# Kernel tuning notes

Hardware: AMD Instinct MI355X
Metric: run time of the kernel (lower is better)

## Reference

```python
import jax, jax.numpy as jnp
import numpy as np

N_ITER = 3  # routing iterations (init kwarg n_iter)


def _squash_elemwise(s):
    # Original squash sums squares over dim=-1, but s_j has a trailing
    # singleton dim there, so it degenerates to an elementwise map:
    # s^2/(1+s^2) * s/|s| == s*|s|/(1+s^2).
    return s * jnp.abs(s) / (1.0 + s * s)


def setup_inputs() -> dict:
    key = jax.random.key(0)
    k1, k2 = jax.random.split(key)
    B, R, C, O, I = 256, 1152, 10, 16, 8
    x = jax.random.normal(k1, (B, R, I), dtype=jnp.float32)
    W = jax.random.normal(k2, (R, C, O, I), dtype=jnp.float32)  # nn.Parameter (leading 1 dropped)
    return {"x": x, "W": W}


def reference(x, W):
    # u_hat[b,r,c,o] = sum_i W[r,c,o,i] * x[b,r,i]
    u_hat = jnp.einsum('rcoi,bri->brco', W, x)  # [B,R,C,O]
    R, C = u_hat.shape[1], u_hat.shape[2]
    b = jnp.zeros((R, C), dtype=u_hat.dtype)  # routing logits, shared across batch
    v = None
    for it in range(N_ITER):
        c = jax.nn.softmax(b, axis=0)                     # softmax over routes (dim=1 orig)
        s = jnp.einsum('rc,brco->bco', c, u_hat)          # weighted sum over routes
        v = _squash_elemwise(s)                           # [B,C,O]
        if it < N_ITER - 1:
            # agreement, mean over batch (b_ij is [1,R,C,1] in original)
            b = b + jnp.einsum('brco,bco->brc', u_hat, v).mean(axis=0)
    return v[..., None]  # matches v_j.squeeze(1): [B, n_capsules, out_ch, 1]
```

## Files before the change

kernel.cpp:

```cpp
#include <hip/hip_runtime.h>
#include <math.h>

namespace {
constexpr int NB = 256;
constexpr int NR = 1152;
constexpr int NC = 10;
constexpr int NO = 16;
constexpr int NI = 8;
constexpr int K1 = NR * NI;
constexpr int NN = NC * NO;
constexpr int KS = 8;
constexpr int KC = K1 / KS;
constexpr int RPB = NR / KS;
}

using s16x8 = __attribute__((ext_vector_type(8))) short;
using f32x4 = __attribute__((ext_vector_type(4))) float;

__device__ __forceinline__ ushort f2bf(float f) {
    uint u = __float_as_uint(f);
    uint r = (u + 0x7FFFu + ((u >> 16) & 1u)) >> 16;
    return (ushort)r;
}

__device__ __forceinline__ s16x8 pack8(float4 a0, float4 a1) {
    s16x8 r;
    r[0] = (short)f2bf(a0.x); r[1] = (short)f2bf(a0.y);
    r[2] = (short)f2bf(a0.z); r[3] = (short)f2bf(a0.w);
    r[4] = (short)f2bf(a1.x); r[5] = (short)f2bf(a1.y);
    r[6] = (short)f2bf(a1.z); r[7] = (short)f2bf(a1.w);
    return r;
}

__device__ __forceinline__ s16x8 pack8s(float4 a0, float4 a1, float cr) {
    s16x8 r;
    r[0] = (short)f2bf(a0.x * cr); r[1] = (short)f2bf(a0.y * cr);
    r[2] = (short)f2bf(a0.z * cr); r[3] = (short)f2bf(a0.w * cr);
    r[4] = (short)f2bf(a1.x * cr); r[5] = (short)f2bf(a1.y * cr);
    r[6] = (short)f2bf(a1.z * cr); r[7] = (short)f2bf(a1.w * cr);
    return r;
}

template <bool FIRST>
__global__ __launch_bounds__(256) void k_a(const float* __restrict__ x,
                                           const float* __restrict__ W,
                                           ushort* __restrict__ Wb,
                                           const float* __restrict__ bbuf,
                                           float* __restrict__ spart,
                                           ushort* __restrict__ xTbf) {
    const int m0 = blockIdx.x * 16;
    const int c  = blockIdx.y;
    const int ks = blockIdx.z;
    const int tid = threadIdx.x;
    const int w = tid >> 6, l = tid & 63;

    __shared__ float red[4][16][16];
    __shared__ float crs[RPB];
    __shared__ float sred[4], sred2[4];

    if constexpr (FIRST) {
        __shared__ __align__(16) ushort T[32][264];
        const int bid = blockIdx.x + 16 * blockIdx.y + 160 * blockIdx.z;
        if (bid < K1 / 32) {
            const int k0 = bid * 32;
            #pragma unroll
            for (int j = 0; j < 8; ++j) {
                int f  = j * 256 + tid;
                int b  = f >> 3;
                int i4 = f & 7;
                float4 v = *reinterpret_cast<const float4*>(
                    x + (size_t)b * K1 + k0 + i4 * 4);
                T[i4 * 4 + 0][b] = f2bf(v.x);
                T[i4 * 4 + 1][b] = f2bf(v.y);
                T[i4 * 4 + 2][b] = f2bf(v.z);
                T[i4 * 4 + 3][b] = f2bf(v.w);
            }
            __syncthreads();
            #pragma unroll
            for (int j = 0; j < 4; ++j) {
                int g   = j * 256 + tid;
                int row = g >> 5;
                int q8  = g & 31;
                *reinterpret_cast<uint4*>(xTbf + (size_t)(k0 + row) * NB + q8 * 8) =
                    *reinterpret_cast<const uint4*>(&T[row][q8 * 8]);
            }
        }
        const int nblk = 16 * NC * KS;
        for (size_t e = (size_t)(blockIdx.x + 16 * blockIdx.y + 160 * blockIdx.z) * 256 + tid;
             e < (size_t)NR * NC * NO; e += (size_t)nblk * 256) {
            float4 v0 = *reinterpret_cast<const float4*>(W + e * 8);
            float4 v1 = *reinterpret_cast<const float4*>(W + e * 8 + 4);
            s16x8 p = pack8(v0, v1);
            *reinterpret_cast<uint4*>(Wb + e * 8) = *reinterpret_cast<uint4*>(&p);
        }
    } else {
        float m = -1e30f;
        for (int r = tid; r < NR; r += 256) m = fmaxf(m, bbuf[r * NC + c]);
        #pragma unroll
        for (int off = 1; off < 64; off <<= 1) m = fmaxf(m, __shfl_xor(m, off));
        if (l == 0) sred[w] = m;
        __syncthreads();
        m = fmaxf(fmaxf(sred[0], sred[1]), fmaxf(sred[2], sred[3]));
        float s = 0.0f;
        for (int r = tid; r < NR; r += 256) s += expf(bbuf[r * NC + c] - m);
        #pragma unroll
        for (int off = 1; off < 64; off <<= 1) s += __shfl_xor(s, off);
        if (l == 0) sred2[w] = s;
        __syncthreads();
        s = sred2[0] + sred2[1] + sred2[2] + sred2[3];
        const float inv = 1.0f / s;
        for (int i = tid; i < RPB; i += 256)
            crs[i] = expf(bbuf[(ks * RPB + i) * NC + c] - m) * inv;
        __syncthreads();
    }

    const int kb = ks * KC + w * (KC / 4);
    const int lg = l >> 4;
    const float* ap = x + (size_t)(m0 + (l & 15)) * K1 + kb + 8 * lg;

    f32x4 acc = {0.f, 0.f, 0.f, 0.f};
    #pragma unroll
    for (int kk = 0; kk < KC / 4 / 32; ++kk) {
        const int k = kb + kk * 32 + 8 * lg;
        const int r = k >> 3;
        float4 a0 = *reinterpret_cast<const float4*>(ap + kk * 32);
        float4 a1 = *reinterpret_cast<const float4*>(ap + kk * 32 + 4);
        const float cr = FIRST ? (1.0f / NR) : crs[r - ks * RPB];
        s16x8 a = pack8s(a0, a1, cr);
        s16x8 b;
        if constexpr (FIRST) {
            const float* wp = W + ((size_t)r * NC + c) * 128 + (l & 15) * 8;
            b = pack8(*reinterpret_cast<const float4*>(wp),
                      *reinterpret_cast<const float4*>(wp + 4));
        } else {
            b = *reinterpret_cast<const s16x8*>(
                Wb + ((size_t)r * NC + c) * 128 + (l & 15) * 8);
        }
        acc = __builtin_amdgcn_mfma_f32_16x16x32_bf16(a, b, acc, 0, 0, 0);
    }

    #pragma unroll
    for (int q = 0; q < 4; ++q) red[w][4 * lg + q][l & 15] = acc[q];
    __syncthreads();
    const int row = tid >> 4, col = tid & 15;
    float s2 = red[0][row][col] + red[1][row][col]
             + red[2][row][col] + red[3][row][col];
    spart[(size_t)ks * (NB * NN) + (size_t)(m0 + row) * NN + c * NO + col] = s2;
}

__global__ __launch_bounds__(256) void k_b(const ushort* __restrict__ xTbf,
                                           const float* __restrict__ spart,
                                           const float* __restrict__ W,
                                           float* __restrict__ bbuf,
                                           int it) {
    const int c = blockIdx.y;
    const int tid = threadIdx.x;
    const int w = tid >> 6, l = tid & 63;

    __shared__ __align__(16) ushort VT[16][264];

    for (int f = tid; f < NB * NO; f += 256) {
        int b  = f >> 4;
        int oo = f & 15;
        size_t idx = (size_t)b * NN + c * NO + oo;
        float s = 0.0f;
        #pragma unroll
        for (int ks = 0; ks < KS; ++ks) s += spart[(size_t)ks * NB * NN + idx];
        float v = s * fabsf(s) / (1.0f + s * s);
        VT[oo][b] = f2bf(v);
    }
    __syncthreads();

    #pragma unroll
    for (int t = 0; t < 4; ++t) {
        const int mt = blockIdx.x * 16 + w * 4 + t;
        const int m0 = mt * 16;
        const ushort* ap = xTbf + (size_t)(m0 + (l & 15)) * NB + 8 * (l >> 4);
        f32x4 acc = {0.f, 0.f, 0.f, 0.f};
        #pragma unroll
        for (int kk = 0; kk < NB / 32; ++kk) {
            s16x8 a = *reinterpret_cast<const s16x8*>(ap + kk * 32);
            s16x8 b = *reinterpret_cast<const s16x8*>(&VT[l & 15][32 * kk + 8 * (l >> 4)]);
            acc = __builtin_amdgcn_mfma_f32_16x16x32_bf16(a, b, acc, 0, 0, 0);
        }
        const int h  = l >> 4, o = l & 15;
        const int r  = (m0 >> 3) + (h >> 1);
        const int i0 = (4 * h) & 7;
        const float4 w4 = *reinterpret_cast<const float4*>(
            W + (((size_t)r * NC + c) * NO + o) * NI + i0);
        float s = acc[0] * w4.x + acc[1] * w4.y + acc[2] * w4.z + acc[3] * w4.w;
        s += __shfl_xor(s, 1);
        s += __shfl_xor(s, 2);
        s += __shfl_xor(s, 4);
        s += __shfl_xor(s, 8);
        s += __shfl_xor(s, 16);
        if (l == 0 || l == 32) {
            int rr = (m0 >> 3) + (l >> 5);
            float val = s * (1.0f / NB);
            if (it > 0) bbuf[(size_t)rr * NC + c] += val;
            else        bbuf[(size_t)rr * NC + c] = val;
        }
    }
}

__global__ __launch_bounds__(256) void k_bf(const float* __restrict__ spart,
                                            float* __restrict__ out) {
    const int m0 = blockIdx.x * 16;
    const int c  = blockIdx.y;
    const int row = threadIdx.x >> 4, col = threadIdx.x & 15;
    size_t idx = (size_t)(m0 + row) * NN + c * NO + col;
    float s = 0.0f;
    #pragma unroll
    for (int ks = 0; ks < KS; ++ks) s += spart[(size_t)ks * NB * NN + idx];
    out[idx] = s * fabsf(s) / (1.0f + s * s);
}

extern "C" void kernel_launch(void* const* d_in, const int* in_sizes, int n_in,
                              void* d_out, int out_size, void* d_ws, size_t ws_size,
                              hipStream_t stream) {
    const float* x = (const float*)d_in[0];
    const float* W = (const float*)d_in[1];
    float* out = (float*)d_out;

    float*  spart = (float*)d_ws;
    float*  bbuf  = spart + (size_t)KS * NB * NN;
    ushort* xTbf  = (ushort*)(bbuf + (size_t)NR * NC);
    ushort* Wb    = xTbf + (size_t)K1 * NB;

    dim3 ga(NB / 16, NC, KS);
    dim3 gb(36, NC);
    dim3 gf(NB / 16, NC);

    k_a<true><<<ga, 256, 0, stream>>>(x, W, Wb, nullptr, spart, xTbf);
    k_b<<<gb, 256, 0, stream>>>(xTbf, spart, W, bbuf, 0);
    k_a<false><<<ga, 256, 0, stream>>>(x, W, Wb, bbuf, spart, nullptr);
    k_b<<<gb, 256, 0, stream>>>(xTbf, spart, W, bbuf, 1);
    k_a<false><<<ga, 256, 0, stream>>>(x, W, Wb, bbuf, spart, nullptr);
    k_bf<<<gf, 256, 0, stream>>>(spart, out);
}
```

Measured before the change: 88.34 us.

## Fuse all routing stages into one persistent kernel with grid barriers

Replaces the six kernel launches with a single persistent kernel of 512 blocks that moves between stages through atomic-counter grid barriers, with the counter reset by a memset before launch. Softmax statistics are now computed per block for all capsules, and the per-route exp is evaluated inline rather than staged in shared memory. Separate spart and bbuf buffers per iteration avoid read-write races across barriers. This removes launch gaps and the tail of each small kernel. The cost is spin-wait barriers, which need all blocks co-resident, and redundant softmax work in every block.

```diff
diff --git a/kernel.cpp b/kernel.cpp
--- a/kernel.cpp
+++ b/kernel.cpp
@@ -11,7 +11,9 @@
 constexpr int NN = NC * NO;
 constexpr int KS = 8;
 constexpr int KC = K1 / KS;
-constexpr int RPB = NR / KS;
+constexpr int SLICE = NB * NN;
+constexpr int GRID = 512;
+constexpr int NTILE1 = 16 * NC * KS;
 }
 
 using s16x8 = __attribute__((ext_vector_type(8))) short;
@@ -41,79 +43,36 @@
     return r;
 }
 
-template <bool FIRST>
-__global__ __launch_bounds__(256) void k_a(const float* __restrict__ x,
-                                           const float* __restrict__ W,
-                                           ushort* __restrict__ Wb,
-                                           const float* __restrict__ bbuf,
-                                           float* __restrict__ spart,
-                                           ushort* __restrict__ xTbf) {
-    const int m0 = blockIdx.x * 16;
-    const int c  = blockIdx.y;
-    const int ks = blockIdx.z;
-    const int tid = threadIdx.x;
-    const int w = tid >> 6, l = tid & 63;
-
-    __shared__ float red[4][16][16];
-    __shared__ float crs[RPB];
-    __shared__ float sred[4], sred2[4];
-
-    if constexpr (FIRST) {
-        __shared__ __align__(16) ushort T[32][264];
-        const int bid = blockIdx.x + 16 * blockIdx.y + 160 * blockIdx.z;
-        if (bid < K1 / 32) {
-            const int k0 = bid * 32;
-            #pragma unroll
-            for (int j = 0; j < 8; ++j) {
-                int f  = j * 256 + tid;
-                int b  = f >> 3;
-                int i4 = f & 7;
-                float4 v = *reinterpret_cast<const float4*>(
-                    x + (size_t)b * K1 + k0 + i4 * 4);
-                T[i4 * 4 + 0][b] = f2bf(v.x);
-                T[i4 * 4 + 1][b] = f2bf(v.y);
-                T[i4 * 4 + 2][b] = f2bf(v.z);
-                T[i4 * 4 + 3][b] = f2bf(v.w);
-            }
-            __syncthreads();
-            #pragma unroll
-            for (int j = 0; j < 4; ++j) {
-                int g   = j * 256 + tid;
-                int row = g >> 5;
-                int q8  = g & 31;
-                *reinterpret_cast<uint4*>(xTbf + (size_t)(k0 + row) * NB + q8 * 8) =
-                    *reinterpret_cast<const uint4*>(&T[row][q8 * 8]);
-            }
-        }
-        const int nblk = 16 * NC * KS;
-        for (size_t e = (size_t)(blockIdx.x + 16 * blockIdx.y + 160 * blockIdx.z) * 256 + tid;
-             e < (size_t)NR * NC * NO; e += (size_t)nblk * 256) {
-            float4 v0 = *reinterpret_cast<const float4*>(W + e * 8);
-            float4 v1 = *reinterpret_cast<const float4*>(W + e * 8 + 4);
-            s16x8 p = pack8(v0, v1);
-            *reinterpret_cast<uint4*>(Wb + e * 8) = *reinterpret_cast<uint4*>(&p);
-        }
-    } else {
-        float m = -1e30f;
-        for (int r = tid; r < NR; r += 256) m = fmaxf(m, bbuf[r * NC + c]);
-        #pragma unroll
-        for (int off = 1; off < 64; off <<= 1) m = fmaxf(m, __shfl_xor(m, off));
-        if (l == 0) sred[w] = m;
-        __syncthreads();
-        m = fmaxf(fmaxf(sred[0], sred[1]), fmaxf(sred[2], sred[3]));
-        float s = 0.0f;
-        for (int r = tid; r < NR; r += 256) s += expf(bbuf[r * NC + c] - m);
-        #pragma unroll
-        for (int off = 1; off < 64; off <<= 1) s += __shfl_xor(s, off);
-        if (l == 0) sred2[w] = s;
-        __syncthreads();
-        s = sred2[0] + sred2[1] + sred2[2] + sred2[3];
-        const float inv = 1.0f / s;
-        for (int i = tid; i < RPB; i += 256)
-            crs[i] = expf(bbuf[(ks * RPB + i) * NC + c] - m) * inv;
-        __syncthreads();
-    }
-
+__device__ __forceinline__ void gbar(unsigned* ctr, unsigned target) {
+    __syncthreads();
+    if (threadIdx.x == 0) {
+        __hip_atomic_fetch_add(ctr, 1u, __ATOMIC_RELEASE, __HIP_MEMORY_SCOPE_AGENT);
+        while (__hip_atomic_load(ctr, __ATOMIC_RELAXED, __HIP_MEMORY_SCOPE_AGENT) < target)
+            __builtin_amdgcn_s_sleep(2);
+        (void)__hip_atomic_load(ctr, __ATOMIC_ACQUIRE, __HIP_MEMORY_SCOPE_AGENT);
+    }
+    __syncthreads();
+}
+
+struct Shm {
+    ushort T[32][264];
+    float  red[4][16][16];
+    ushort VT[16][264];
+    float  smM[NC], smI[NC];
+};
+
+__device__ __forceinline__ void ka_tile(int j, int it,
+                                        const float* __restrict__ x,
+                                        const float* __restrict__ W,
+                                        const ushort* __restrict__ Wb,
+                                        const float* __restrict__ bb,
+                                        float* __restrict__ sp,
+                                        Shm* sh, int tid, int w, int l) {
+    const int mt = j & 15;
+    const int rest = j >> 4;
+    const int c  = rest % NC;
+    const int ks = rest / NC;
+    const int m0 = mt * 16;
     const int kb = ks * KC + w * (KC / 4);
     const int lg = l >> 4;
     const float* ap = x + (size_t)(m0 + (l & 15)) * K1 + kb + 8 * lg;
@@ -125,10 +84,12 @@
         const int r = k >> 3;
         float4 a0 = *reinterpret_cast<const float4*>(ap + kk * 32);
         float4 a1 = *reinterpret_cast<const float4*>(ap + kk * 32 + 4);
-        const float cr = FIRST ? (1.0f / NR) : crs[r - ks * RPB];
+        float cr;
+        if (it == 0) cr = 1.0f / NR;
+        else         cr = expf(bb[r * NC + c] - sh->smM[c]) * sh->smI[c];
         s16x8 a = pack8s(a0, a1, cr);
         s16x8 b;
-        if constexpr (FIRST) {
+        if (it == 0) {
             const float* wp = W + ((size_t)r * NC + c) * 128 + (l & 15) * 8;
             b = pack8(*reinterpret_cast<const float4*>(wp),
                       *reinterpret_cast<const float4*>(wp + 4));
@@ -139,25 +100,25 @@
         acc = __builtin_amdgcn_mfma_f32_16x16x32_bf16(a, b, acc, 0, 0, 0);
     }
 
+    __syncthreads();
     #pragma unroll
-    for (int q = 0; q < 4; ++q) red[w][4 * lg + q][l & 15] = acc[q];
+    for (int q = 0; q < 4; ++q) sh->red[w][4 * lg + q][l & 15] = acc[q];
     __syncthreads();
     const int row = tid >> 4, col = tid & 15;
-    float s2 = red[0][row][col] + red[1][row][col]
-             + red[2][row][col] + red[3][row][col];
-    spart[(size_t)ks * (NB * NN) + (size_t)(m0 + row) * NN + c * NO + col] = s2;
-}
-
-__global__ __launch_bounds__(256) void k_b(const ushort* __restrict__ xTbf,
-                                           const float* __restrict__ spart,
-                                           const float* __restrict__ W,
-                                           float* __restrict__ bbuf,
-                                           int it) {
-    const int c = blockIdx.y;
-    const int tid = threadIdx.x;
-    const int w = tid >> 6, l = tid & 63;
-
-    __shared__ __align__(16) ushort VT[16][264];
+    float s2 = sh->red[0][row][col] + sh->red[1][row][col]
+             + sh->red[2][row][col] + sh->red[3][row][col];
+    sp[(size_t)ks * SLICE + (size_t)(m0 + row) * NN + c * NO + col] = s2;
+}
+
+__device__ __forceinline__ void b_tile(int jx,
+                                       const ushort* __restrict__ xTbf,
+                                       const float* __restrict__ sp,
+                                       const float* __restrict__ W,
+                                       const float* __restrict__ bbR,
+                                       float* __restrict__ bbW,
+                                       Shm* sh, int tid, int w, int l) {
+    const int c = jx % NC;
+    const int jm = jx / NC;
 
     for (int f = tid; f < NB * NO; f += 256) {
         int b  = f >> 4;
@@ -165,22 +126,23 @@
         size_t idx = (size_t)b * NN + c * NO + oo;
         float s = 0.0f;
         #pragma unroll
-        for (int ks = 0; ks < KS; ++ks) s += spart[(size_t)ks * NB * NN + idx];
+        for (int ks = 0; ks < KS; ++ks) s += sp[(size_t)ks * SLICE + idx];
         float v = s * fabsf(s) / (1.0f + s * s);
-        VT[oo][b] = f2bf(v);
+        sh->VT[oo][b] = f2bf(v);
     }
     __syncthreads();
 
     #pragma unroll
     for (int t = 0; t < 4; ++t) {
-        const int mt = blockIdx.x * 16 + w * 4 + t;
+        const int mt = jm * 16 + w * 4 + t;
         const int m0 = mt * 16;
         const ushort* ap = xTbf + (size_t)(m0 + (l & 15)) * NB + 8 * (l >> 4);
         f32x4 acc = {0.f, 0.f, 0.f, 0.f};
         #pragma unroll
         for (int kk = 0; kk < NB / 32; ++kk) {
             s16x8 a = *reinterpret_cast<const s16x8*>(ap + kk * 32);
-            s16x8 b = *reinterpret_cast<const s16x8*>(&VT[l & 15][32 * kk + 8 * (l >> 4)]);
+            s16x8 b = *reinterpret_cast<const s16x8*>(
+                &sh->VT[l & 15][32 * kk + 8 * (l >> 4)]);
             acc = __builtin_amdgcn_mfma_f32_16x16x32_bf16(a, b, acc, 0, 0, 0);
         }
         const int h  = l >> 4, o = l & 15;
@@ -197,22 +159,109 @@
         if (l == 0 || l == 32) {
             int rr = (m0 >> 3) + (l >> 5);
             float val = s * (1.0f / NB);
-            if (it > 0) bbuf[(size_t)rr * NC + c] += val;
-            else        bbuf[(size_t)rr * NC + c] = val;
-        }
-    }
-}
-
-__global__ __launch_bounds__(256) void k_bf(const float* __restrict__ spart,
-                                            float* __restrict__ out) {
-    const int m0 = blockIdx.x * 16;
-    const int c  = blockIdx.y;
-    const int row = threadIdx.x >> 4, col = threadIdx.x & 15;
-    size_t idx = (size_t)(m0 + row) * NN + c * NO + col;
-    float s = 0.0f;
-    #pragma unroll
-    for (int ks = 0; ks < KS; ++ks) s += spart[(size_t)ks * NB * NN + idx];
-    out[idx] = s * fabsf(s) / (1.0f + s * s);
+            bbW[(size_t)rr * NC + c] = (bbR ? bbR[(size_t)rr * NC + c] : 0.0f) + val;
+        }
+    }
+    __syncthreads();
+}
+
+__device__ __forceinline__ void smax_stats(const float* __restrict__ bb,
+                                           Shm* sh, int w, int l) {
+    for (int c = w; c < NC; c += 4) {
+        float m = -1e30f;
+        for (int r = l; r < NR; r += 64) m = fmaxf(m, bb[r * NC + c]);
+        #pragma unroll
+        for (int off = 1; off < 64; off <<= 1) m = fmaxf(m, __shfl_xor(m, off));
+        float s = 0.0f;
+        for (int r = l; r < NR; r += 64) s += expf(bb[r * NC + c] - m);
+        #pragma unroll
+        for (int off = 1; off < 64; off <<= 1) s += __shfl_xor(s, off);
+        if (l == 0) { sh->smM[c] = m; sh->smI[c] = 1.0f / s; }
+    }
+    __syncthreads();
+}
+
+__global__ __launch_bounds__(256, 2) void k_all(const float* __restrict__ x,
+                                                const float* __restrict__ W,
+                                                float* __restrict__ out,
+                                                unsigned* __restrict__ ctr,
+                                                float* __restrict__ spart,
+                                                float* __restrict__ bbuf0,
+                                                float* __restrict__ bbuf1,
+                                                ushort* __restrict__ xTbf,
+                                                ushort* __restrict__ Wb) {
+    const int bid = blockIdx.x;
+    const int tid = threadIdx.x;
+    const int w = tid >> 6, l = tid & 63;
+    __shared__ Shm sh;
+
+    float* sp0 = spart;
+    float* sp1 = spart + (size_t)KS * SLICE;
+    float* sp2 = spart + (size_t)2 * KS * SLICE;
+
+    for (int j = bid; j < K1 / 32; j += GRID) {
+        const int k0 = j * 32;
+        #pragma unroll
+        for (int jj = 0; jj < 8; ++jj) {
+            int f  = jj * 256 + tid;
+            int b  = f >> 3;
+            int i4 = f & 7;
+            float4 v = *reinterpret_cast<const float4*>(
+                x + (size_t)b * K1 + k0 + i4 * 4);
+            sh.T[i4 * 4 + 0][b] = f2bf(v.x);
+            sh.T[i4 * 4 + 1][b] = f2bf(v.y);
+            sh.T[i4 * 4 + 2][b] = f2bf(v.z);
+            sh.T[i4 * 4 + 3][b] = f2bf(v.w);
+        }
+        __syncthreads();
+        #pragma unroll
+        for (int jj = 0; jj < 4; ++jj) {
+            int g   = jj * 256 + tid;
+            int row = g >> 5;
+            int q8  = g & 31;
+            *reinterpret_cast<uint4*>(xTbf + (size_t)(k0 + row) * NB + q8 * 8) =
+                *reinterpret_cast<const uint4*>(&sh.T[row][q8 * 8]);
+        }
+        __syncthreads();
+    }
+    for (size_t e = (size_t)bid * 256 + tid; e < (size_t)NR * NC * NO;
+         e += (size_t)GRID * 256) {
+        float4 v0 = *reinterpret_cast<const float4*>(W + e * 8);
+        float4 v1 = *reinterpret_cast<const float4*>(W + e * 8 + 4);
+        s16x8 p = pack8(v0, v1);
+        *reinterpret_cast<uint4*>(Wb + e * 8) = *reinterpret_cast<uint4*>(&p);
+    }
+    for (int j = bid; j < NTILE1; j += GRID)
+        ka_tile(j, 0, x, W, Wb, nullptr, sp0, &sh, tid, w, l);
+    gbar(ctr, GRID);
+
+    if (bid < 360) b_tile(bid, xTbf, sp0, W, nullptr, bbuf0, &sh, tid, w, l);
+    gbar(ctr, 2 * GRID);
+
+    smax_stats(bbuf0, &sh, w, l);
+    for (int j = bid; j < NTILE1; j += GRID)
+        ka_tile(j, 1, x, W, Wb, bbuf0, sp1, &sh, tid, w, l);
+    gbar(ctr, 3 * GRID);
+
+    if (bid < 360) b_tile(bid, xTbf, sp1, W, bbuf0, bbuf1, &sh, tid, w, l);
+    gbar(ctr, 4 * GRID);
+
+    smax_stats(bbuf1, &sh, w, l);
+    for (int j = bid; j < NTILE1; j += GRID)
+        ka_tile(j, 2, x, W, Wb, bbuf1, sp2, &sh, tid, w, l);
+    gbar(ctr, 5 * GRID);
+
+    if (bid < 160) {
+        const int mt = bid & 15;
+        const int c  = bid >> 4;
+        const int m0 = mt * 16;
+        const int row = tid >> 4, col = tid & 15;
+        size_t idx = (size_t)(m0 + row) * NN + c * NO + col;
+        float s = 0.0f;
+        #pragma unroll
+        for (int ks = 0; ks < KS; ++ks) s += sp2[(size_t)ks * SLICE + idx];
+        out[idx] = s * fabsf(s) / (1.0f + s * s);
+    }
 }
 
 extern "C" void kernel_launch(void* const* d_in, const int* in_sizes, int n_in,
@@ -222,19 +271,13 @@
     const float* W = (const float*)d_in[1];
     float* out = (float*)d_out;
 
-    float*  spart = (float*)d_ws;
-    float*  bbuf  = spart + (size_t)KS * NB * NN;
-    ushort* xTbf  = (ushort*)(bbuf + (size_t)NR * NC);
-    ushort* Wb    = xTbf + (size_t)K1 * NB;
-
-    dim3 ga(NB / 16, NC, KS);
-    dim3 gb(36, NC);
-    dim3 gf(NB / 16, NC);
-
-    k_a<true><<<ga, 256, 0, stream>>>(x, W, Wb, nullptr, spart, xTbf);
-    k_b<<<gb, 256, 0, stream>>>(xTbf, spart, W, bbuf, 0);
-    k_a<false><<<ga, 256, 0, stream>>>(x, W, Wb, bbuf, spart, nullptr);
-    k_b<<<gb, 256, 0, stream>>>(xTbf, spart, W, bbuf, 1);
-    k_a<false><<<ga, 256, 0, stream>>>(x, W, Wb, bbuf, spart, nullptr);
-    k_bf<<<gf, 256, 0, stream>>>(spart, out);
-}
+    unsigned* ctr  = (unsigned*)d_ws;
+    float*  spart  = (float*)((char*)d_ws + 256);
+    float*  bbuf0  = spart + (size_t)3 * KS * SLICE;
+    float*  bbuf1  = bbuf0 + (size_t)NR * NC;
+    ushort* xTbf   = (ushort*)(bbuf1 + (size_t)NR * NC);
+    ushort* Wb     = xTbf + (size_t)K1 * NB;
+
+    hipMemsetAsync(ctr, 0, 256, stream);
+    k_all<<<GRID, 256, 0, stream>>>(x, W, out, ctr, spart, bbuf0, bbuf1, xTbf, Wb);
+}
```

After: 326.4 us. 269% more time.
